# Optimization experiments

Measured on AMD Instinct MI355X. Metric: run time of the kernel, lower is better.

## Reference

```python
import jax, jax.numpy as jnp
import numpy as np
from jax import lax

D_MODEL = 1024
D_STATE = 16


def setup_inputs() -> dict:
    key = jax.random.key(0)
    ks = jax.random.split(key, 7)
    B, L = 4, 2048
    x = jax.random.normal(ks[0], (B, L, D_MODEL), dtype=jnp.float32)
    s = 1.0 / np.sqrt(D_MODEL)
    W_dt = jax.random.uniform(ks[1], (D_MODEL, D_MODEL), jnp.float32, -s, s)
    b_dt = jax.random.uniform(ks[2], (D_MODEL,), jnp.float32, -s, s)
    W_B = jax.random.uniform(ks[3], (D_STATE, D_MODEL), jnp.float32, -s, s)
    W_C = jax.random.uniform(ks[4], (D_STATE, D_MODEL), jnp.float32, -s, s)
    A = jax.random.normal(ks[5], (D_MODEL, D_STATE), dtype=jnp.float32)
    A_log = jnp.log(jnp.abs(A) + 1e-4)
    D = jnp.ones((D_MODEL,), dtype=jnp.float32)
    return {"x": x, "W_dt": W_dt, "b_dt": b_dt, "W_B": W_B, "W_C": W_C,
            "A_log": A_log, "D": D}


def reference(x, W_dt, b_dt, W_B, W_C, A_log, D):
    B, L, Dm = x.shape
    N = A_log.shape[1]
    dt = jax.nn.softplus(jnp.einsum('bld,ed->ble', x, W_dt) + b_dt)  # [B,L,D]
    Bp = jnp.einsum('bld,nd->bln', x, W_B)   # [B,L,N]
    Cp = jnp.einsum('bld,nd->bln', x, W_C)   # [B,L,N]
    A = -jnp.exp(A_log)                      # [D,N]
    dA = jnp.exp(dt[..., None] * A)          # [B,L,D,N]
    # fuse dB * x: dB[bldn] = dt*Bp; input term = dB * x
    dBx = dt[..., None] * Bp[:, :, None, :] * x[..., None]  # [B,L,D,N]

    def step(h, inp):
        dA_t, dBx_t, C_t, x_t = inp
        h = dA_t * h + dBx_t                              # [B,D,N]
        y = jnp.einsum('bdn,bn->bd', h, C_t) + D * x_t    # [B,D]
        return h, y

    h0 = jnp.zeros((B, Dm, N), dtype=x.dtype)
    xs = (jnp.swapaxes(dA, 0, 1), jnp.swapaxes(dBx, 0, 1),
          jnp.swapaxes(Cp, 0, 1), jnp.swapaxes(x, 0, 1))
    _, ys = lax.scan(step, h0, xs)           # ys: [L,B,D]
    return jnp.swapaxes(ys, 0, 1)            # [B,L,D]
```

## Files before the change

kernel.cpp:

```cpp
#include <hip/hip_runtime.h>
#include <hip/hip_bf16.h>
#include <math.h>

#define DM 1024
#define DS 16
#define BB 4
#define LL 2048
#define LC 32
#define NC (LL/LC)
#define MT 8192
#define NT64 16
#define NCT 17

typedef __attribute__((ext_vector_type(8))) short short8;
typedef __attribute__((ext_vector_type(4))) float floatx4;

__device__ __forceinline__ float softplus_fast(float v) {
  return fmaxf(v, 0.f) + __logf(1.f + __expf(-fabsf(v)));
}

__global__ __launch_bounds__(256) void convert_kernel(
    const float* __restrict__ X, const float* __restrict__ W_dt,
    const float* __restrict__ WB, const float* __restrict__ WC,
    __hip_bfloat16* __restrict__ Xb, __hip_bfloat16* __restrict__ Wx)
{
  const size_t i  = (size_t)blockIdx.x * 256 + threadIdx.x;
  const size_t NX = (size_t)MT * DM / 8;
  const size_t NW = (size_t)DM * DM / 8;
  const size_t NB = (size_t)DS * DM / 8;
  const float* src;
  __hip_bfloat16* dst;
  size_t u;
  if (i < NX)                { src = X;    dst = Xb;                        u = i; }
  else if (i < NX + NW)      { src = W_dt; dst = Wx;                        u = i - NX; }
  else if (i < NX + NW + NB) { src = WB;   dst = Wx + (size_t)1024 * DM;    u = i - NX - NW; }
  else if (i < NX + NW + 2 * NB) { src = WC; dst = Wx + (size_t)1040 * DM;  u = i - NX - NW - NB; }
  else {
    const size_t z = i - NX - NW - 2 * NB;
    const short8 zz = {0, 0, 0, 0, 0, 0, 0, 0};
    *(short8*)&Wx[(size_t)1056 * DM + z * 8] = zz;
    return;
  }
  const float4 a = *(const float4*)&src[u * 8];
  const float4 b = *(const float4*)&src[u * 8 + 4];
  union { short8 v; __hip_bfloat16 h[8]; } o;
  o.h[0] = __float2bfloat16(a.x); o.h[1] = __float2bfloat16(a.y);
  o.h[2] = __float2bfloat16(a.z); o.h[3] = __float2bfloat16(a.w);
  o.h[4] = __float2bfloat16(b.x); o.h[5] = __float2bfloat16(b.y);
  o.h[6] = __float2bfloat16(b.z); o.h[7] = __float2bfloat16(b.w);
  *(short8*)&dst[u * 8] = o.v;
}

__global__ __launch_bounds__(512, 4) void gemm_dt_mfma(
    const __hip_bfloat16* __restrict__ Xb, const __hip_bfloat16* __restrict__ Wx,
    const float* __restrict__ bias, __hip_bfloat16* __restrict__ DTb,
    float* __restrict__ BP, float* __restrict__ CP)
{
  __shared__ short As[2][256 * 64];
  __shared__ short Bs[2][64 * 64];
  const int tid  = threadIdx.x;
  const int lane = tid & 63;
  const int wid  = tid >> 6;
  const int wm   = wid >> 1, wn = wid & 1;

  const int bid  = blockIdx.x;
  const int tile = (bid & 7) * 68 + (bid >> 3);
  const int row0 = (tile / NCT) * 256;
  const int col0 = (tile % NCT) * 64;

  const floatx4 zero = {0.f, 0.f, 0.f, 0.f};
  floatx4 acc[4][2];
#pragma unroll
  for (int i = 0; i < 4; ++i)
#pragma unroll
    for (int j = 0; j < 2; ++j) acc[i][j] = zero;

  auto STAGE = [&](int buf, int t) {
    const int k0 = t * 64;
#pragma unroll
    for (int q = 0; q < 4; ++q) {
      const int fe = q * 512 + tid;
      const int r  = fe >> 3;
      const int kk = (fe & 7) ^ (r & 7);
      __builtin_amdgcn_global_load_lds(
          (const __attribute__((address_space(1))) void*)&Xb[(size_t)(row0 + r) * DM + k0 + kk * 8],
          (__attribute__((address_space(3))) void*)&As[buf][fe * 8], 16, 0, 0);
    }
    {
      const int fe = tid;
      const int r  = fe >> 3;
      const int kk = (fe & 7) ^ (r & 7);
      __builtin_amdgcn_global_load_lds(
          (const __attribute__((address_space(1))) void*)&Wx[(size_t)(col0 + r) * DM + k0 + kk * 8],
          (__attribute__((address_space(3))) void*)&Bs[buf][fe * 8], 16, 0, 0);
    }
  };

  const int fr = lane & 15;
  const int ks = lane >> 4;

  STAGE(0, 0);
  int cur = 0;
  for (int t = 0; t < NT64; ++t) {
    if (t + 1 < NT64) {
      STAGE(cur ^ 1, t + 1);
      asm volatile("s_waitcnt vmcnt(5)" ::: "memory");
    } else {
      asm volatile("s_waitcnt vmcnt(0)" ::: "memory");
    }
    __builtin_amdgcn_s_barrier();
    __builtin_amdgcn_sched_barrier(0);

    short8 af[4][2], bfr[2][2];
#pragma unroll
    for (int i = 0; i < 4; ++i) {
      const int ar = wm * 64 + i * 16 + fr;
#pragma unroll
      for (int s = 0; s < 2; ++s) {
        const int ch = (ks + 4 * s) ^ (ar & 7);
        af[i][s] = *(const short8*)&As[cur][ar * 64 + ch * 8];
      }
    }
#pragma unroll
    for (int j = 0; j < 2; ++j) {
      const int br = wn * 32 + j * 16 + fr;
#pragma unroll
      for (int s = 0; s < 2; ++s) {
        const int ch = (ks + 4 * s) ^ (br & 7);
        bfr[j][s] = *(const short8*)&Bs[cur][br * 64 + ch * 8];
      }
    }
    __builtin_amdgcn_s_setprio(1);
#pragma unroll
    for (int s = 0; s < 2; ++s)
#pragma unroll
      for (int i = 0; i < 4; ++i)
#pragma unroll
        for (int j = 0; j < 2; ++j)
          acc[i][j] = __builtin_amdgcn_mfma_f32_16x16x32_bf16(af[i][s], bfr[j][s], acc[i][j], 0, 0, 0);
    __builtin_amdgcn_s_setprio(0);
    __builtin_amdgcn_sched_barrier(0);

    if (t + 1 < NT64) {
      __builtin_amdgcn_s_barrier();
      cur ^= 1;
    }
  }

  const int cl = lane & 15;
  const int rg = lane >> 4;
  if (col0 < 1024) {
#pragma unroll
    for (int i = 0; i < 4; ++i) {
#pragma unroll
      for (int r = 0; r < 4; ++r) {
        const size_t row = (size_t)(row0 + wm * 64 + i * 16 + rg * 4 + r);
#pragma unroll
        for (int j = 0; j < 2; ++j) {
          const int col = col0 + wn * 32 + j * 16 + cl;
          const float v = acc[i][j][r] + bias[col];
          DTb[row * DM + col] = __float2bfloat16(softplus_fast(v));
        }
      }
    }
  } else if (wn == 0) {
#pragma unroll
    for (int i = 0; i < 4; ++i) {
#pragma unroll
      for (int r = 0; r < 4; ++r) {
        const size_t row = (size_t)(row0 + wm * 64 + i * 16 + rg * 4 + r);
        BP[row * DS + cl] = acc[i][0][r];
        CP[row * DS + cl] = acc[i][1][r];
      }
    }
  }
}

__global__ __launch_bounds__(256) void scan_partial_kernel(
    const __hip_bfloat16* __restrict__ DT, const __hip_bfloat16* __restrict__ X,
    const float* __restrict__ Bp, const float* __restrict__ A_log,
    float* __restrict__ SD, float* __restrict__ HP)
{
  __shared__ float sB[LC * DS];
  const int tid = threadIdx.x;
  const int d  = blockIdx.x * 128 + (tid >> 1);
  const int nh = tid & 1;
  const int c = blockIdx.y;
  const int b = blockIdx.z;
  const int l0 = c * LC;

  if (tid < LC * DS / 4)
    ((float4*)sB)[tid] = ((const float4*)&Bp[((size_t)b * LL + l0) * DS])[tid];

  float A[8], h[8];
  float sdt = 0.f;
  const float4* arow = (const float4*)&A_log[(size_t)d * DS + nh * 8];
  {
    const float4 a0 = arow[0], a1 = arow[1];
    A[0]=-__expf(a0.x); A[1]=-__expf(a0.y); A[2]=-__expf(a0.z); A[3]=-__expf(a0.w);
    A[4]=-__expf(a1.x); A[5]=-__expf(a1.y); A[6]=-__expf(a1.z); A[7]=-__expf(a1.w);
  }
#pragma unroll
  for (int n = 0; n < 8; ++n) h[n] = 0.f;

  size_t idx = ((size_t)b * LL + l0) * DM + d;
  float dtb[4], xb[4];
#pragma unroll
  for (int u = 0; u < 4; ++u) {
    dtb[u] = __bfloat162float(DT[idx + (size_t)u * DM]);
    xb[u]  = __bfloat162float(X[idx + (size_t)u * DM]);
  }
  __syncthreads();

  for (int l = 0; l < LC; l += 4) {
    float dtn[4], xn[4];
    if (l + 4 < LC) {
#pragma unroll
      for (int u = 0; u < 4; ++u) {
        dtn[u] = __bfloat162float(DT[idx + (size_t)(u + 4) * DM]);
        xn[u]  = __bfloat162float(X[idx + (size_t)(u + 4) * DM]);
      }
    }
#pragma unroll
    for (int u = 0; u < 4; ++u) {
      const float dtv = dtb[u], xv = xb[u];
      const float dx = dtv * xv;
      sdt += dtv;
      const float4 b0 = ((const float4*)sB)[(l+u)*4 + nh*2 + 0];
      const float4 b1 = ((const float4*)sB)[(l+u)*4 + nh*2 + 1];
      const float bb[8] = {b0.x,b0.y,b0.z,b0.w, b1.x,b1.y,b1.z,b1.w};
#pragma unroll
      for (int n = 0; n < 8; ++n) {
        const float dA = __expf(dtv * A[n]);
        h[n] = fmaf(dA, h[n], dx * bb[n]);
      }
    }
    idx += (size_t)4 * DM;
#pragma unroll
    for (int u = 0; u < 4; ++u) { dtb[u] = dtn[u]; xb[u] = xn[u]; }
  }
  if (nh == 0) SD[((size_t)b * NC + c) * DM + d] = sdt;
  const size_t o = (((size_t)b * NC + c) * DM + d) * DS + nh * 8;
  float4* hp = (float4*)&HP[o];
  hp[0] = make_float4(h[0], h[1], h[2], h[3]);
  hp[1] = make_float4(h[4], h[5], h[6], h[7]);
}

__global__ __launch_bounds__(256) void combine_kernel(
    const float* __restrict__ SD, const float* __restrict__ A_log,
    float* HP)
{
  const int idx = blockIdx.x * 256 + threadIdx.x;
  const int b  = idx >> 14;
  const int dn = idx & 16383;
  const int d  = dn >> 4;
  const float A = -__expf(A_log[dn]);
  float h = 0.f;
#pragma unroll 4
  for (int c = 0; c < NC; ++c) {
    const size_t o = (((size_t)b * NC + c) << 14) + dn;
    const float p  = __expf(SD[((size_t)b * NC + c) * DM + d] * A);
    const float hp = HP[o];
    HP[o] = h;
    h = fmaf(p, h, hp);
  }
}

__global__ __launch_bounds__(256) void scan_final_kernel(
    const __hip_bfloat16* __restrict__ DT, const __hip_bfloat16* __restrict__ X,
    const float* __restrict__ Bp, const float* __restrict__ Cp,
    const float* __restrict__ A_log, const float* __restrict__ Dvec,
    const float* __restrict__ Hin, float* __restrict__ Y)
{
  __shared__ float sB[LC * DS], sC[LC * DS];
  const int tid = threadIdx.x;
  const int d  = blockIdx.x * 128 + (tid >> 1);
  const int nh = tid & 1;
  const int c = blockIdx.y;
  const int b = blockIdx.z;
  const int l0 = c * LC;

  if (tid < 128)  ((float4*)sB)[tid] = ((const float4*)&Bp[((size_t)b * LL + l0) * DS])[tid];
  else            ((float4*)sC)[tid - 128] = ((const float4*)&Cp[((size_t)b * LL + l0) * DS])[tid - 128];

  float A[8], h[8];
  const float4* arow = (const float4*)&A_log[(size_t)d * DS + nh * 8];
  {
    const float4 a0 = arow[0], a1 = arow[1];
    A[0]=-__expf(a0.x); A[1]=-__expf(a0.y); A[2]=-__expf(a0.z); A[3]=-__expf(a0.w);
    A[4]=-__expf(a1.x); A[5]=-__expf(a1.y); A[6]=-__expf(a1.z); A[7]=-__expf(a1.w);
  }
  const size_t o = (((size_t)b * NC + c) * DM + d) * DS + nh * 8;
  {
    const float4 h0 = ((const float4*)&Hin[o])[0];
    const float4 h1 = ((const float4*)&Hin[o])[1];
    h[0]=h0.x; h[1]=h0.y; h[2]=h0.z; h[3]=h0.w;
    h[4]=h1.x; h[5]=h1.y; h[6]=h1.z; h[7]=h1.w;
  }
  const float Dd = Dvec[d];
  size_t idx = ((size_t)b * LL + l0) * DM + d;

  float dtb[4], xb[4];
#pragma unroll
  for (int u = 0; u < 4; ++u) {
    dtb[u] = __bfloat162float(DT[idx + (size_t)u * DM]);
    xb[u]  = __bfloat162float(X[idx + (size_t)u * DM]);
  }
  __syncthreads();

  for (int l = 0; l < LC; l += 4) {
    float dtn[4], xn[4];
    if (l + 4 < LC) {
#pragma unroll
      for (int u = 0; u < 4; ++u) {
        dtn[u] = __bfloat162float(DT[idx + (size_t)(u + 4) * DM]);
        xn[u]  = __bfloat162float(X[idx + (size_t)(u + 4) * DM]);
      }
    }
#pragma unroll
    for (int u = 0; u < 4; ++u) {
      const float dtv = dtb[u], xv = xb[u];
      const float dx = dtv * xv;
      const float4 b0 = ((const float4*)sB)[(l+u)*4 + nh*2 + 0];
      const float4 b1 = ((const float4*)sB)[(l+u)*4 + nh*2 + 1];
      const float bb[8] = {b0.x,b0.y,b0.z,b0.w, b1.x,b1.y,b1.z,b1.w};
      const float4 c0 = ((const float4*)sC)[(l+u)*4 + nh*2 + 0];
      const float4 c1 = ((const float4*)sC)[(l+u)*4 + nh*2 + 1];
      const float cc[8] = {c0.x,c0.y,c0.z,c0.w, c1.x,c1.y,c1.z,c1.w};
      float y = 0.f;
#pragma unroll
      for (int n = 0; n < 8; ++n) {
        const float dA = __expf(dtv * A[n]);
        h[n] = fmaf(dA, h[n], dx * bb[n]);
        y = fmaf(h[n], cc[n], y);
      }
      y += __shfl_xor(y, 1, 64);
      if (nh == 0) Y[idx + (size_t)u * DM] = fmaf(Dd, xv, y);
    }
    idx += (size_t)4 * DM;
#pragma unroll
    for (int u = 0; u < 4; ++u) { dtb[u] = dtn[u]; xb[u] = xn[u]; }
  }
}

extern "C" void kernel_launch(void* const* d_in, const int* in_sizes, int n_in,
                              void* d_out, int out_size, void* d_ws, size_t ws_size,
                              hipStream_t stream)
{
  const float* x     = (const float*)d_in[0];
  const float* W_dt  = (const float*)d_in[1];
  const float* b_dt  = (const float*)d_in[2];
  const float* W_B   = (const float*)d_in[3];
  const float* W_C   = (const float*)d_in[4];
  const float* A_log = (const float*)d_in[5];
  const float* Dv    = (const float*)d_in[6];
  float* Y  = (float*)d_out;
  float* ws = (float*)d_ws;

  __hip_bfloat16* DTb = (__hip_bfloat16*)ws;
  float* BP = ws + (size_t)MT * DM / 2;
  float* CP = BP + (size_t)MT * DS;
  __hip_bfloat16* Xb = (__hip_bfloat16*)(CP + (size_t)MT * DS);
  __hip_bfloat16* Wx = (__hip_bfloat16*)(CP + (size_t)MT * DS + (size_t)MT * DM / 2);
  float* SD = CP + (size_t)MT * DS + (size_t)MT * DM / 2 + (size_t)1088 * DM / 2;
  float* HP = SD + (size_t)BB * NC * DM;

  convert_kernel<<<4640, 256, 0, stream>>>(x, W_dt, W_B, W_C, Xb, Wx);
  gemm_dt_mfma<<<544, 512, 0, stream>>>(Xb, Wx, b_dt, DTb, BP, CP);
  scan_partial_kernel<<<dim3(DM * 2 / 256, NC, BB), 256, 0, stream>>>(DTb, Xb, BP, A_log, SD, HP);
  combine_kernel<<<(BB * DM * DS) / 256, 256, 0, stream>>>(SD, A_log, HP);
  scan_final_kernel<<<dim3(DM * 2 / 256, NC, BB), 256, 0, stream>>>(DTb, Xb, BP, CP, A_log, Dv, HP, Y);
}
```

Measured before the change: 119.1 us.

## Store dt and x transposed (channel-major) for scans, bf16 chunk states

The convert kernel now also writes a transposed bf16 copy of x through a shared-memory tile, and the GEMM epilogue writes softplus(dt) transposed (channel-major) with 4-element packed stores. The scan kernels then read 8 consecutive timesteps per channel in one 16-byte load instead of strided 2-byte loads. Chunk carry states are stored as bf16 instead of fp32 to cut traffic in the partial, combine and final passes. The cost is an extra 16 MB transposed x write, partial-line scattered stores in the GEMM epilogue, and lower precision for the carried states.

```diff
diff --git a/kernel.cpp b/kernel.cpp
--- a/kernel.cpp
+++ b/kernel.cpp
@@ -13,30 +13,66 @@
 #define NCT 17
 
 typedef __attribute__((ext_vector_type(8))) short short8;
+typedef __attribute__((ext_vector_type(4))) short short4v;
 typedef __attribute__((ext_vector_type(4))) float floatx4;
 
 __device__ __forceinline__ float softplus_fast(float v) {
   return fmaxf(v, 0.f) + __logf(1.f + __expf(-fabsf(v)));
+}
+__device__ __forceinline__ float bf2f(short s) {
+  union { short s2[2]; float f; } u; u.s2[0] = 0; u.s2[1] = s; return u.f;
 }
 
 __global__ __launch_bounds__(256) void convert_kernel(
     const float* __restrict__ X, const float* __restrict__ W_dt,
     const float* __restrict__ WB, const float* __restrict__ WC,
-    __hip_bfloat16* __restrict__ Xb, __hip_bfloat16* __restrict__ Wx)
-{
-  const size_t i  = (size_t)blockIdx.x * 256 + threadIdx.x;
-  const size_t NX = (size_t)MT * DM / 8;
+    __hip_bfloat16* __restrict__ Xb, __hip_bfloat16* __restrict__ XbT,
+    __hip_bfloat16* __restrict__ Wx)
+{
+  const int tid = threadIdx.x;
+  if (blockIdx.x < 2048) {
+    __shared__ __hip_bfloat16 tile[64 * 65];
+    const int tb = blockIdx.x;
+    const int t0 = (tb & 127) * 64;
+    const int d0 = (tb >> 7) * 64;
+    const int tr  = tid >> 4;
+    const int tc4 = (tid & 15) * 4;
+#pragma unroll
+    for (int p = 0; p < 4; ++p) {
+      const int row = p * 16 + tr;
+      const float4 v = *(const float4*)&X[(size_t)(t0 + row) * DM + d0 + tc4];
+      union { short4v v4; __hip_bfloat16 h[4]; } pk;
+      pk.h[0] = __float2bfloat16(v.x); pk.h[1] = __float2bfloat16(v.y);
+      pk.h[2] = __float2bfloat16(v.z); pk.h[3] = __float2bfloat16(v.w);
+      tile[row * 65 + tc4 + 0] = pk.h[0];
+      tile[row * 65 + tc4 + 1] = pk.h[1];
+      tile[row * 65 + tc4 + 2] = pk.h[2];
+      tile[row * 65 + tc4 + 3] = pk.h[3];
+      *(short4v*)&Xb[(size_t)(t0 + row) * DM + d0 + tc4] = pk.v4;
+    }
+    __syncthreads();
+#pragma unroll
+    for (int p = 0; p < 4; ++p) {
+      const int drow = p * 16 + tr;
+      union { short4v v4; __hip_bfloat16 h[4]; } pk;
+#pragma unroll
+      for (int q = 0; q < 4; ++q)
+        pk.h[q] = tile[(tc4 + q) * 65 + drow];
+      *(short4v*)&XbT[(size_t)(d0 + drow) * MT + t0 + tc4] = pk.v4;
+    }
+    return;
+  }
+  const size_t u0 = (size_t)(blockIdx.x - 2048) * 256 + tid;
   const size_t NW = (size_t)DM * DM / 8;
   const size_t NB = (size_t)DS * DM / 8;
   const float* src;
   __hip_bfloat16* dst;
   size_t u;
-  if (i < NX)                { src = X;    dst = Xb;                        u = i; }
-  else if (i < NX + NW)      { src = W_dt; dst = Wx;                        u = i - NX; }
-  else if (i < NX + NW + NB) { src = WB;   dst = Wx + (size_t)1024 * DM;    u = i - NX - NW; }
-  else if (i < NX + NW + 2 * NB) { src = WC; dst = Wx + (size_t)1040 * DM;  u = i - NX - NW - NB; }
+  if (u0 < NW)           { src = W_dt; dst = Wx;                       u = u0; }
+  else if (u0 < NW + NB) { src = WB;   dst = Wx + (size_t)1024 * DM;   u = u0 - NW; }
+  else if (u0 < NW + 2 * NB) { src = WC; dst = Wx + (size_t)1040 * DM; u = u0 - NW - NB; }
   else {
-    const size_t z = i - NX - NW - 2 * NB;
+    const size_t z = u0 - NW - 2 * NB;
     const short8 zz = {0, 0, 0, 0, 0, 0, 0, 0};
     *(short8*)&Wx[(size_t)1056 * DM + z * 8] = zz;
     return;
@@ -53,7 +89,7 @@
 
 __global__ __launch_bounds__(512, 4) void gemm_dt_mfma(
     const __hip_bfloat16* __restrict__ Xb, const __hip_bfloat16* __restrict__ Wx,
-    const float* __restrict__ bias, __hip_bfloat16* __restrict__ DTb,
+    const float* __restrict__ bias, __hip_bfloat16* __restrict__ DTt,
     float* __restrict__ BP, float* __restrict__ CP)
 {
   __shared__ short As[2][256 * 64];
@@ -152,15 +188,15 @@
   if (col0 < 1024) {
 #pragma unroll
     for (int i = 0; i < 4; ++i) {
-#pragma unroll
-      for (int r = 0; r < 4; ++r) {
-        const size_t row = (size_t)(row0 + wm * 64 + i * 16 + rg * 4 + r);
-#pragma unroll
-        for (int j = 0; j < 2; ++j) {
-          const int col = col0 + wn * 32 + j * 16 + cl;
-          const float v = acc[i][j][r] + bias[col];
-          DTb[row * DM + col] = __float2bfloat16(softplus_fast(v));
-        }
+      const size_t rowbase = (size_t)(row0 + wm * 64 + i * 16 + rg * 4);
+#pragma unroll
+      for (int j = 0; j < 2; ++j) {
+        const int col = col0 + wn * 32 + j * 16 + cl;
+        union { short4v v4; __hip_bfloat16 h[4]; } pk;
+#pragma unroll
+        for (int r = 0; r < 4; ++r)
+          pk.h[r] = __float2bfloat16(softplus_fast(acc[i][j][r] + bias[col]));
+        *(short4v*)&DTt[(size_t)col * MT + rowbase] = pk.v4;
       }
     }
   } else if (wn == 0) {
@@ -177,9 +213,9 @@
 }
 
 __global__ __launch_bounds__(256) void scan_partial_kernel(
-    const __hip_bfloat16* __restrict__ DT, const __hip_bfloat16* __restrict__ X,
+    const __hip_bfloat16* __restrict__ DTt, const __hip_bfloat16* __restrict__ XbT,
     const float* __restrict__ Bp, const float* __restrict__ A_log,
-    float* __restrict__ SD, float* __restrict__ HP)
+    float* __restrict__ SD, __hip_bfloat16* __restrict__ HP)
 {
   __shared__ float sB[LC * DS];
   const int tid = threadIdx.x;
@@ -203,27 +239,21 @@
 #pragma unroll
   for (int n = 0; n < 8; ++n) h[n] = 0.f;
 
-  size_t idx = ((size_t)b * LL + l0) * DM + d;
-  float dtb[4], xb[4];
-#pragma unroll
-  for (int u = 0; u < 4; ++u) {
-    dtb[u] = __bfloat162float(DT[idx + (size_t)u * DM]);
-    xb[u]  = __bfloat162float(X[idx + (size_t)u * DM]);
-  }
+  const __hip_bfloat16* dT = &DTt[(size_t)d * MT + (size_t)b * LL + l0];
+  const __hip_bfloat16* xT = &XbT[(size_t)d * MT + (size_t)b * LL + l0];
+  short8 d8 = *(const short8*)dT;
+  short8 x8 = *(const short8*)xT;
   __syncthreads();
 
-  for (int l = 0; l < LC; l += 4) {
-    float dtn[4], xn[4];
-    if (l + 4 < LC) {
-#pragma unroll
-      for (int u = 0; u < 4; ++u) {
-        dtn[u] = __bfloat162float(DT[idx + (size_t)(u + 4) * DM]);
-        xn[u]  = __bfloat162float(X[idx + (size_t)(u + 4) * DM]);
-      }
-    }
-#pragma unroll
-    for (int u = 0; u < 4; ++u) {
-      const float dtv = dtb[u], xv = xb[u];
+  for (int l = 0; l < LC; l += 8) {
+    short8 d8n, x8n;
+    if (l + 8 < LC) {
+      d8n = *(const short8*)(dT + l + 8);
+      x8n = *(const short8*)(xT + l + 8);
+    }
+#pragma unroll
+    for (int u = 0; u < 8; ++u) {
+      const float dtv = bf2f(d8[u]), xv = bf2f(x8[u]);
       const float dx = dtv * xv;
       sdt += dtv;
       const float4 b0 = ((const float4*)sB)[(l+u)*4 + nh*2 + 0];
@@ -235,20 +265,19 @@
         h[n] = fmaf(dA, h[n], dx * bb[n]);
       }
     }
-    idx += (size_t)4 * DM;
-#pragma unroll
-    for (int u = 0; u < 4; ++u) { dtb[u] = dtn[u]; xb[u] = xn[u]; }
+    d8 = d8n; x8 = x8n;
   }
   if (nh == 0) SD[((size_t)b * NC + c) * DM + d] = sdt;
   const size_t o = (((size_t)b * NC + c) * DM + d) * DS + nh * 8;
-  float4* hp = (float4*)&HP[o];
-  hp[0] = make_float4(h[0], h[1], h[2], h[3]);
-  hp[1] = make_float4(h[4], h[5], h[6], h[7]);
+  union { short8 v; __hip_bfloat16 h[8]; } pk;
+#pragma unroll
+  for (int n = 0; n < 8; ++n) pk.h[n] = __float2bfloat16(h[n]);
+  *(short8*)&HP[o] = pk.v;
 }
 
 __global__ __launch_bounds__(256) void combine_kernel(
     const float* __restrict__ SD, const float* __restrict__ A_log,
-    float* HP)
+    __hip_bfloat16* HP)
 {
   const int idx = blockIdx.x * 256 + threadIdx.x;
   const int b  = idx >> 14;
@@ -260,17 +289,17 @@
   for (int c = 0; c < NC; ++c) {
     const size_t o = (((size_t)b * NC + c) << 14) + dn;
     const float p  = __expf(SD[((size_t)b * NC + c) * DM + d] * A);
-    const float hp = HP[o];
-    HP[o] = h;
+    const float hp = __bfloat162float(HP[o]);
+    HP[o] = __float2bfloat16(h);
     h = fmaf(p, h, hp);
   }
 }
 
 __global__ __launch_bounds__(256) void scan_final_kernel(
-    const __hip_bfloat16* __restrict__ DT, const __hip_bfloat16* __restrict__ X,
+    const __hip_bfloat16* __restrict__ DTt, const __hip_bfloat16* __restrict__ XbT,
     const float* __restrict__ Bp, const float* __restrict__ Cp,
     const float* __restrict__ A_log, const float* __restrict__ Dvec,
-    const float* __restrict__ Hin, float* __restrict__ Y)
+    const __hip_bfloat16* __restrict__ Hin, float* __restrict__ Y)
 {
   __shared__ float sB[LC * DS], sC[LC * DS];
   const int tid = threadIdx.x;
@@ -292,34 +321,27 @@
   }
   const size_t o = (((size_t)b * NC + c) * DM + d) * DS + nh * 8;
   {
-    const float4 h0 = ((const float4*)&Hin[o])[0];
-    const float4 h1 = ((const float4*)&Hin[o])[1];
-    h[0]=h0.x; h[1]=h0.y; h[2]=h0.z; h[3]=h0.w;
-    h[4]=h1.x; h[5]=h1.y; h[6]=h1.z; h[7]=h1.w;
+    const short8 hv = *(const short8*)&Hin[o];
+#pragma unroll
+    for (int n = 0; n < 8; ++n) h[n] = bf2f(hv[n]);
   }
   const float Dd = Dvec[d];
-  size_t idx = ((size_t)b * LL + l0) * DM + d;
-
-  float dtb[4], xb[4];
-#pragma unroll
-  for (int u = 0; u < 4; ++u) {
-    dtb[u] = __bfloat162float(DT[idx + (size_t)u * DM]);
-    xb[u]  = __bfloat162float(X[idx + (size_t)u * DM]);
-  }
+  const size_t tok0 = (size_t)b * LL + l0;
+  const __hip_bfloat16* dT = &DTt[(size_t)d * MT + tok0];
+  const __hip_bfloat16* xT = &XbT[(size_t)d * MT + tok0];
+  short8 d8 = *(const short8*)dT;
+  short8 x8 = *(const short8*)xT;
   __syncthreads();
 
-  for (int l = 0; l < LC; l += 4) {
-    float dtn[4], xn[4];
-    if (l + 4 < LC) {
-#pragma unroll
-      for (int u = 0; u < 4; ++u) {
-        dtn[u] = __bfloat162float(DT[idx + (size_t)(u + 4) * DM]);
-        xn[u]  = __bfloat162float(X[idx + (size_t)(u + 4) * DM]);
-      }
-    }
-#pragma unroll
-    for (int u = 0; u < 4; ++u) {
-      const float dtv = dtb[u], xv = xb[u];
+  for (int l = 0; l < LC; l += 8) {
+    short8 d8n, x8n;
+    if (l + 8 < LC) {
+      d8n = *(const short8*)(dT + l + 8);
+      x8n = *(const short8*)(xT + l + 8);
+    }
+#pragma unroll
+    for (int u = 0; u < 8; ++u) {
+      const float dtv = bf2f(d8[u]), xv = bf2f(x8[u]);
       const float dx = dtv * xv;
       const float4 b0 = ((const float4*)sB)[(l+u)*4 + nh*2 + 0];
       const float4 b1 = ((const float4*)sB)[(l+u)*4 + nh*2 + 1];
@@ -335,11 +357,9 @@
         y = fmaf(h[n], cc[n], y);
       }
       y += __shfl_xor(y, 1, 64);
-      if (nh == 0) Y[idx + (size_t)u * DM] = fmaf(Dd, xv, y);
-    }
-    idx += (size_t)4 * DM;
-#pragma unroll
-    for (int u = 0; u < 4; ++u) { dtb[u] = dtn[u]; xb[u] = xn[u]; }
+      if (nh == 0) Y[(tok0 + l + u) * DM + d] = fmaf(Dd, xv, y);
+    }
+    d8 = d8n; x8 = x8n;
   }
 }
 
@@ -357,17 +377,18 @@
   float* Y  = (float*)d_out;
   float* ws = (float*)d_ws;
 
-  __hip_bfloat16* DTb = (__hip_bfloat16*)ws;
+  __hip_bfloat16* DTt = (__hip_bfloat16*)ws;
   float* BP = ws + (size_t)MT * DM / 2;
   float* CP = BP + (size_t)MT * DS;
-  __hip_bfloat16* Xb = (__hip_bfloat16*)(CP + (size_t)MT * DS);
-  __hip_bfloat16* Wx = (__hip_bfloat16*)(CP + (size_t)MT * DS + (size_t)MT * DM / 2);
-  float* SD = CP + (size_t)MT * DS + (size_t)MT * DM / 2 + (size_t)1088 * DM / 2;
-  float* HP = SD + (size_t)BB * NC * DM;
-
-  convert_kernel<<<4640, 256, 0, stream>>>(x, W_dt, W_B, W_C, Xb, Wx);
-  gemm_dt_mfma<<<544, 512, 0, stream>>>(Xb, Wx, b_dt, DTb, BP, CP);
-  scan_partial_kernel<<<dim3(DM * 2 / 256, NC, BB), 256, 0, stream>>>(DTb, Xb, BP, A_log, SD, HP);
+  __hip_bfloat16* Xb  = (__hip_bfloat16*)(CP + (size_t)MT * DS);
+  __hip_bfloat16* XbT = Xb + (size_t)MT * DM;
+  __hip_bfloat16* Wx  = XbT + (size_t)MT * DM;
+  float* SD = (float*)(Wx + (size_t)1088 * DM);
+  __hip_bfloat16* HP = (__hip_bfloat16*)(SD + (size_t)BB * NC * DM);
+
+  convert_kernel<<<2592, 256, 0, stream>>>(x, W_dt, W_B, W_C, Xb, XbT, Wx);
+  gemm_dt_mfma<<<544, 512, 0, stream>>>(Xb, Wx, b_dt, DTt, BP, CP);
+  scan_partial_kernel<<<dim3(DM * 2 / 256, NC, BB), 256, 0, stream>>>(DTt, XbT, BP, A_log, SD, HP);
   combine_kernel<<<(BB * DM * DS) / 256, 256, 0, stream>>>(SD, A_log, HP);
-  scan_final_kernel<<<dim3(DM * 2 / 256, NC, BB), 256, 0, stream>>>(DTb, Xb, BP, CP, A_log, Dv, HP, Y);
-}
+  scan_final_kernel<<<dim3(DM * 2 / 256, NC, BB), 256, 0, stream>>>(DTt, XbT, BP, CP, A_log, Dv, HP, Y);
+}
```

Result: no change. 119.1 us (-0.0%).
